# Kernel tuning notes

Hardware: AMD Instinct MI355X
Metric: run time of the kernel (lower is better)

The kernel has to match this reference:

```python
import jax, jax.numpy as jnp
import numpy as np

EPS = 1e-06
NUM_HEADS = 16
THETA = 10000.0


def rope_tables(grid_size, head_dim):
    # matches VisionRotaryEmbeddingFast: 2D rope, table shape [grid^2, head_dim]
    half = head_dim // 2
    freqs = 1.0 / THETA ** (jnp.arange(0, half, 2, dtype=jnp.float32) / half)
    freqs = jnp.concatenate([freqs, freqs], axis=0)  # [half]
    t = jnp.arange(grid_size, dtype=jnp.float32)
    f = jnp.outer(t, freqs)  # [grid, half]
    fh = jnp.broadcast_to(f[:, None, :], (grid_size, grid_size, half))
    fw = jnp.broadcast_to(f[None, :, :], (grid_size, grid_size, half))
    full = jnp.concatenate([fh, fw], axis=-1).reshape(-1, head_dim)  # [N, head_dim]
    return jnp.cos(full), jnp.sin(full)


def rotate_half(x):
    n = x.shape[-1] // 2
    return jnp.concatenate((-x[..., n:], x[..., :n]), axis=-1)


def rms_norm(x, gamma):
    var = jnp.mean(x * x, axis=-1, keepdims=True)
    return x * jax.lax.rsqrt(var + EPS) * gamma


def setup_inputs() -> dict:
    key = jax.random.key(0)
    ks = jax.random.split(key, 5)
    B, N, C = 32, 1024, 1024
    return {
        "x": jax.random.normal(ks[0], (B, N, C), dtype=jnp.float32),
        "qkv_w": jax.random.normal(ks[1], (C, 3 * C), dtype=jnp.float32) * (C ** -0.5),
        "qkv_b": jnp.zeros((3 * C,), dtype=jnp.float32),
        "proj_w": jax.random.normal(ks[2], (C, C), dtype=jnp.float32) * (C ** -0.5),
        "proj_b": jnp.zeros((C,), dtype=jnp.float32),
        "q_gamma": jnp.ones((C // NUM_HEADS,), dtype=jnp.float32),
        "k_gamma": jnp.ones((C // NUM_HEADS,), dtype=jnp.float32),
    }


def reference(x, qkv_w, qkv_b, proj_w, proj_b, q_gamma, k_gamma):
    B, N, C = x.shape
    H = NUM_HEADS
    hd = C // H
    grid = int(np.sqrt(N))
    cos, sin = rope_tables(grid, hd)  # [N, hd] each
    cos = cos[None, :, None, :]  # broadcast over [B, N, H, hd]
    sin = sin[None, :, None, :]

    qkv = (x @ qkv_w + qkv_b).reshape(B, N, 3, H, hd)
    q, k, v = qkv[:, :, 0], qkv[:, :, 1], qkv[:, :, 2]  # [B, N, H, hd]

    q = rms_norm(q, q_gamma)
    k = rms_norm(k, k_gamma)
    q = q * cos + rotate_half(q) * sin
    k = k * cos + rotate_half(k) * sin

    out = jax.nn.dot_product_attention(q, k, v, is_causal=False)  # [B, N, H, hd]
    out = out.reshape(B, N, C)
    return out @ proj_w + proj_b
```

## Files before the change

### kernel.cpp

```cpp
#include <hip/hip_runtime.h>
#include <stdint.h>

typedef float f32x4 __attribute__((ext_vector_type(4)));
typedef short s16x8 __attribute__((ext_vector_type(8)));
typedef unsigned short u16;

__device__ __forceinline__ u16 f2bf(float f) {
  union { float f; uint32_t u; } c; c.f = f;
  uint32_t u = c.u;
  u = (u + 0x7fffu + ((u >> 16) & 1u)) >> 16;
  return (u16)u;
}

__device__ __forceinline__ u16 f2bf_fast(float f) {
  union { float f; uint32_t u; } c; c.f = f;
  return (u16)((c.u + 0x8000u) >> 16);
}

__device__ __forceinline__ void gload16(const void* g, void* lds) {
  __builtin_amdgcn_global_load_lds(
      (const __attribute__((address_space(1))) void*)g,
      (__attribute__((address_space(3))) void*)lds, 16, 0, 0);
}

__device__ __forceinline__ f32x4 mfma16(s16x8 a, s16x8 b, f32x4 c) {
  return __builtin_amdgcn_mfma_f32_16x16x32_bf16(a, b, c, 0, 0, 0);
}

__device__ __forceinline__ int swz(int row, int c8) {
  return row * 64 + ((c8 ^ (row & 7)) << 3);
}

__global__ void cvt_bf16(const float* __restrict__ in, u16* __restrict__ out, size_t n) {
  size_t i = ((size_t)blockIdx.x * blockDim.x + threadIdx.x) * 4;
  if (i < n) {
    float4 v = *(const float4*)&in[i];
    u16 o0 = f2bf(v.x), o1 = f2bf(v.y), o2 = f2bf(v.z), o3 = f2bf(v.w);
    uint2 packed;
    packed.x = (uint32_t)o0 | ((uint32_t)o1 << 16);
    packed.y = (uint32_t)o2 | ((uint32_t)o3 << 16);
    *(uint2*)&out[i] = packed;
  }
}

__global__ void transpose_cvt(const float* __restrict__ in, u16* __restrict__ out,
                              int rows, int cols) {
  __shared__ float tile[64][65];
  const int c0 = blockIdx.x * 64, r0 = blockIdx.y * 64;
  const int tr = threadIdx.x >> 6, tc = threadIdx.x & 63;
#pragma unroll
  for (int i = 0; i < 16; i++) {
    int r = i * 4 + tr;
    tile[r][tc] = in[(size_t)(r0 + r) * cols + c0 + tc];
  }
  __syncthreads();
#pragma unroll
  for (int i = 0; i < 16; i++) {
    int oc = i * 4 + tr;
    out[(size_t)(c0 + oc) * rows + r0 + tc] = f2bf(tile[tc][oc]);
  }
}

__global__ void rope_tables_kernel(float* __restrict__ cosT, float* __restrict__ sinT) {
  int n = blockIdx.x;
  int d = threadIdx.x;
  int ph = n >> 5, pw = n & 31;
  int pos = (d < 32) ? ph : pw;
  int fi = d & 15;
  float freq = powf(10000.f, -(float)fi / 16.f);
  float ang = (float)pos * freq;
  cosT[n * 64 + d] = cosf(ang);
  sinT[n * 64 + d] = sinf(ang);
}


#define PH_MID \
  __builtin_amdgcn_sched_barrier(0); \
  __builtin_amdgcn_s_barrier(); \
  asm volatile("s_waitcnt lgkmcnt(0)" ::: "memory"); \
  __builtin_amdgcn_sched_barrier(0); \
  __builtin_amdgcn_s_setprio(1);

#define PH_END \
  __builtin_amdgcn_s_setprio(0); \
  __builtin_amdgcn_sched_barrier(0); \
  __builtin_amdgcn_s_barrier(); \
  __builtin_amdgcn_sched_barrier(0);

#define STAGE(ldsoff, g) do { \
    gload16((g) + (size_t)(w8 + srow) * 1024 + sc8 * 8,       &lds[(ldsoff) + w8 * 64]); \
    gload16((g) + (size_t)(w8 + srow + 64) * 1024 + sc8 * 8,  &lds[(ldsoff) + (w8 + 64) * 64]); \
  } while (0)

#define RD_A(dst, BUF, mh) \
  _Pragma("unroll") \
  for (int mi = 0; mi < 4; mi++) { \
    dst[mi][0] = *(const s16x8*)&lds[(BUF) * 32768 + arow0 + ((mh) * 64 + mi * 16) * 64 + swz0]; \
    dst[mi][1] = *(const s16x8*)&lds[(BUF) * 32768 + arow0 + ((mh) * 64 + mi * 16) * 64 + swz1]; \
  }

#define RD_B(dst, BUF, nh) \
  _Pragma("unroll") \
  for (int ni = 0; ni < 2; ni++) { \
    dst[ni][0] = *(const s16x8*)&lds[(BUF) * 32768 + 16384 + brow0 + ((nh) * 32 + ni * 16) * 64 + swz0]; \
    dst[ni][1] = *(const s16x8*)&lds[(BUF) * 32768 + 16384 + brow0 + ((nh) * 32 + ni * 16) * 64 + swz1]; \
  }

#define MFMA_QUAD(af, bfr, mh, nh) \
  _Pragma("unroll") \
  for (int mi = 0; mi < 4; mi++) \
    _Pragma("unroll") \
    for (int ni = 0; ni < 2; ni++) { \
      acc[(mh) * 4 + mi][(nh) * 2 + ni] = mfma16(af[mi][0], bfr[ni][0], acc[(mh) * 4 + mi][(nh) * 2 + ni]); \
      acc[(mh) * 4 + mi][(nh) * 2 + ni] = mfma16(af[mi][1], bfr[ni][1], acc[(mh) * 4 + mi][(nh) * 2 + ni]); \
    }

#define KTILE(BUF, KT, MODE) do { \
    s16x8 a0f[4][2], a1f[4][2], b0f[2][2], b1f[2][2]; \
     \
    RD_A(a0f, BUF, 0); \
    RD_B(b0f, BUF, 0); \
    if ((MODE) < 2) STAGE((1 - (BUF)) * 32768, Ag + (size_t)((KT) + 1) * 64); \
    PH_MID; MFMA_QUAD(a0f, b0f, 0, 0); PH_END; \
     \
    RD_B(b1f, BUF, 1); \
    if ((MODE) < 2) STAGE((1 - (BUF)) * 32768 + 8192, Ag + (size_t)128 * 1024 + ((KT) + 1) * 64); \
    PH_MID; MFMA_QUAD(a0f, b1f, 0, 1); PH_END; \
     \
    RD_A(a1f, BUF, 1); \
    if ((MODE) == 0) STAGE((BUF) * 32768 + 16384, Bg + (size_t)((KT) + 2) * 64); \
    PH_MID; MFMA_QUAD(a1f, b1f, 1, 1); PH_END; \
     \
    if ((MODE) == 0) STAGE((BUF) * 32768 + 16384 + 8192, Bg + (size_t)128 * 1024 + ((KT) + 2) * 64); \
    PH_MID; MFMA_QUAD(a1f, b0f, 1, 0); \
    __builtin_amdgcn_s_setprio(0); \
    if ((MODE) == 0) asm volatile("s_waitcnt vmcnt(4)" ::: "memory"); \
    if ((MODE) == 1) asm volatile("s_waitcnt vmcnt(0)" ::: "memory"); \
    __builtin_amdgcn_sched_barrier(0); \
    __builtin_amdgcn_s_barrier(); \
    __builtin_amdgcn_sched_barrier(0); \
  } while (0)

__device__ __forceinline__ void gemm_mainloop_8ph(
    const u16* __restrict__ Ag, const u16* __restrict__ Bg,
    u16* lds, f32x4 (&acc)[8][4])
{
  const int t = threadIdx.x;
  const int l = t & 63, w = t >> 6;
  const int wm = w & 1, wn = w >> 1;
  const int lrow = l & 15, lg = l >> 4;
  const int srow = l >> 3, sc8 = (l & 7) ^ srow;
  const int w8 = w * 8;
  const int swz0 = ((0 + lg) ^ (lrow & 7)) << 3;
  const int swz1 = ((4 + lg) ^ (lrow & 7)) << 3;
  const int arow0 = (wm * 128 + lrow) * 64;
  const int brow0 = (wn * 64 + lrow) * 64;

  STAGE(0,                 Ag);
  STAGE(8192,              Ag + (size_t)128 * 1024);
  STAGE(16384,             Bg);
  STAGE(16384 + 8192,      Bg + (size_t)128 * 1024);
  STAGE(32768 + 16384,          Bg + 64);
  STAGE(32768 + 16384 + 8192,   Bg + (size_t)128 * 1024 + 64);
  asm volatile("s_waitcnt vmcnt(4)" ::: "memory");
  __builtin_amdgcn_sched_barrier(0);
  __builtin_amdgcn_s_barrier();
  __builtin_amdgcn_sched_barrier(0);

#pragma unroll 1
  for (int kt = 0; kt < 14; kt += 2) {
    KTILE(0, kt, 0);
    KTILE(1, kt + 1, 0);
  }
  KTILE(0, 14, 1);
  KTILE(1, 15, 2);
}

__global__ __launch_bounds__(512, 2) void gemm_qkv(
    const u16* __restrict__ A,
    const u16* __restrict__ Bt,
    const float* __restrict__ bias,
    const float* __restrict__ qgam, const float* __restrict__ kgam,
    const float* __restrict__ cosT, const float* __restrict__ sinT,
    u16* __restrict__ qb, u16* __restrict__ kb, u16* __restrict__ vb)
{
  __shared__ u16 lds[65536];
  const int bid = blockIdx.x;
  const int sb = (bid & 7) * 192 + (bid >> 3);
  const int bm = sb / 12, bn = sb % 12;

  const f32x4 fzero = {0.f, 0.f, 0.f, 0.f};
  f32x4 acc[8][4];
#pragma unroll
  for (int i = 0; i < 8; i++)
#pragma unroll
    for (int j = 0; j < 4; j++) acc[i][j] = fzero;

  gemm_mainloop_8ph(A + (size_t)bm * 256 * 1024, Bt + (size_t)bn * 256 * 1024, lds, acc);

  const int t = threadIdx.x, l = t & 63, w = t >> 6;
  const int wm = w & 1, wn = w >> 1, lrow = l & 15, lg = l >> 4;
  const int colb = bn * 256 + wn * 64;
  const int s = colb >> 10;
  const int h = (colb & 1023) >> 6;

  float biasv[4], g[4];
#pragma unroll
  for (int nt = 0; nt < 4; nt++) biasv[nt] = bias[colb + nt * 16 + lrow];
  const float* gamma = (s == 0) ? qgam : kgam;
#pragma unroll
  for (int nt = 0; nt < 4; nt++) g[nt] = gamma[nt * 16 + lrow];

  if (s < 2) {
    u16* dst = (s == 0) ? qb : kb;
    const float mul = (s == 0) ? 0.18033688011112042f : 1.0f;
#pragma unroll
    for (int mf = 0; mf < 8; mf++) {
#pragma unroll
      for (int r = 0; r < 4; r++) {
        const int rowg = bm * 256 + wm * 128 + mf * 16 + lg * 4 + r;
        const int b = rowg >> 10, np = rowg & 1023;
        float tmp[4]; float sq = 0.f;
#pragma unroll
        for (int nt = 0; nt < 4; nt++) {
          float v = acc[mf][nt][r] + biasv[nt];
          tmp[nt] = v; sq += v * v;
        }
#pragma unroll
        for (int off = 1; off < 16; off <<= 1) sq += __shfl_xor(sq, off);
        const float rstd = rsqrtf(sq * 0.015625f + 1e-6f);
#pragma unroll
        for (int nt = 0; nt < 4; nt++) tmp[nt] *= rstd * g[nt];
        const size_t base = (((size_t)(b * 16 + h)) * 1024 + np) * 64;
#pragma unroll
        for (int nt = 0; nt < 4; nt++) {
          const int d = nt * 16 + lrow;
          const float cv = cosT[np * 64 + d], sv = sinT[np * 64 + d];
          const float rh = (nt < 2) ? -tmp[nt + 2] : tmp[nt - 2];
          dst[base + d] = f2bf((tmp[nt] * cv + rh * sv) * mul);
        }
      }
    }
  } else {
#pragma unroll
    for (int mf = 0; mf < 8; mf++) {
#pragma unroll
      for (int r = 0; r < 4; r++) {
        const int rowg = bm * 256 + wm * 128 + mf * 16 + lg * 4 + r;
        const int b = rowg >> 10, np = rowg & 1023;
        const size_t hb = ((size_t)(b * 16 + h)) * 64;
#pragma unroll
        for (int nt = 0; nt < 4; nt++) {
          const int d = nt * 16 + lrow;
          vb[(hb + d) * 1024 + np] = f2bf(acc[mf][nt][r] + biasv[nt]);
        }
      }
    }
  }
}

__global__ __launch_bounds__(256, 3) void attn_kernel(
    const u16* __restrict__ qbuf, const u16* __restrict__ kbuf,
    const u16* __restrict__ vtbuf, u16* __restrict__ obuf)
{
  __shared__ u16 Qs[128 * 64];
  __shared__ u16 Ks[64 * 64];
  __shared__ u16 VTs[64 * 64];
  __shared__ u16 Ps[128 * 64];
  const int bx = blockIdx.x;
  const int bh = bx >> 3, qt = bx & 7;
  const int t = threadIdx.x, l = t & 63, w = t >> 6;
  const int lrow = l & 15, lg = l >> 4;

  const u16* qg  = qbuf  + (size_t)bh * 65536 + (size_t)qt * 8192;
  const u16* kg0 = kbuf  + (size_t)bh * 65536;
  const u16* vt0 = vtbuf + (size_t)bh * 65536;

  const int srow = l >> 3;
  const int sc8  = (l & 7) ^ (srow & 7);

#pragma unroll
  for (int i = 0; i < 4; i++) {
    const int r0 = (w + i * 4) * 8;
    gload16(qg + (size_t)(r0 + srow) * 64 + sc8 * 8, &Qs[r0 * 64]);
  }
#pragma unroll
  for (int i = 0; i < 2; i++) {
    const int r0 = (w + i * 4) * 8;
    gload16(kg0 + (size_t)(r0 + srow) * 64 + sc8 * 8, &Ks[r0 * 64]);
    gload16(vt0 + (size_t)(r0 + srow) * 1024 + sc8 * 8, &VTs[r0 * 64]);
  }
  asm volatile("s_waitcnt vmcnt(0)" ::: "memory");
  __syncthreads();

  s16x8 aq[2][2];
#pragma unroll
  for (int mt = 0; mt < 2; mt++)
#pragma unroll
    for (int kh = 0; kh < 2; kh++)
      aq[mt][kh] = *(const s16x8*)&Qs[swz(w * 32 + mt * 16 + lrow, kh * 4 + lg)];

  const f32x4 fzero = {0.f, 0.f, 0.f, 0.f};
  f32x4 o[2][4];
  float l_[2][4];
#pragma unroll
  for (int mt = 0; mt < 2; mt++) {
#pragma unroll
    for (int dt = 0; dt < 4; dt++) o[mt][dt] = fzero;
#pragma unroll
    for (int r = 0; r < 4; r++) l_[mt][r] = 0.f;
  }

  for (int kt = 0; kt < 16; kt++) {
    s16x8 bk[4][2];
#pragma unroll
    for (int nt = 0; nt < 4; nt++)
#pragma unroll
      for (int kh = 0; kh < 2; kh++)
        bk[nt][kh] = *(const s16x8*)&Ks[swz(nt * 16 + lrow, kh * 4 + lg)];

    f32x4 sf[2][4];
#pragma unroll
    for (int mt = 0; mt < 2; mt++)
#pragma unroll
      for (int nt = 0; nt < 4; nt++) {
        f32x4 z = fzero;
        z = mfma16(aq[mt][0], bk[nt][0], z);
        z = mfma16(aq[mt][1], bk[nt][1], z);
        sf[mt][nt] = z;
      }

#pragma unroll
    for (int mt = 0; mt < 2; mt++) {
      const int rowb = w * 32 + mt * 16 + lg * 4;
#pragma unroll
      for (int r = 0; r < 4; r++) {
        const int row = rowb + r;
        u16* prow = &Ps[row * 64 + (lrow & 7)];
        const int rm = row & 7;
        float acc_l = 0.f;
#pragma unroll
        for (int nt = 0; nt < 4; nt++) {
          float p = __builtin_amdgcn_exp2f(sf[mt][nt][r]);
          acc_l += p;
          prow[((nt * 2 + (lrow >> 3)) ^ rm) << 3] = f2bf_fast(p);
        }
        l_[mt][r] += acc_l;
      }
    }
    asm volatile("s_waitcnt lgkmcnt(0)" ::: "memory");

    s16x8 ap[2][2], bv[4][2];
#pragma unroll
    for (int mt = 0; mt < 2; mt++)
#pragma unroll
      for (int kh = 0; kh < 2; kh++)
        ap[mt][kh] = *(const s16x8*)&Ps[swz(w * 32 + mt * 16 + lrow, kh * 4 + lg)];
#pragma unroll
    for (int dt = 0; dt < 4; dt++)
#pragma unroll
      for (int kh = 0; kh < 2; kh++)
        bv[dt][kh] = *(const s16x8*)&VTs[swz(dt * 16 + lrow, kh * 4 + lg)];
#pragma unroll
    for (int mt = 0; mt < 2; mt++)
#pragma unroll
      for (int dt = 0; dt < 4; dt++) {
        o[mt][dt] = mfma16(ap[mt][0], bv[dt][0], o[mt][dt]);
        o[mt][dt] = mfma16(ap[mt][1], bv[dt][1], o[mt][dt]);
      }

    __syncthreads();
    if (kt < 15) {
      const int kb = (kt + 1) * 64;
#pragma unroll
      for (int i = 0; i < 2; i++) {
        const int r0 = (w + i * 4) * 8;
        gload16(kg0 + (size_t)(kb + r0 + srow) * 64 + sc8 * 8, &Ks[r0 * 64]);
        gload16(vt0 + (size_t)(r0 + srow) * 1024 + kb + sc8 * 8, &VTs[r0 * 64]);
      }
      asm volatile("s_waitcnt vmcnt(0)" ::: "memory");
      __syncthreads();
    }
  }

  const int b = bh >> 4, h = bh & 15;
#pragma unroll
  for (int mt = 0; mt < 2; mt++)
#pragma unroll
    for (int r = 0; r < 4; r++) {
      float lsum = l_[mt][r];
#pragma unroll
      for (int off = 1; off < 16; off <<= 1) lsum += __shfl_xor(lsum, off);
      const float inv = 1.0f / lsum;
      const int n = qt * 128 + w * 32 + mt * 16 + lg * 4 + r;
      const size_t base = (((size_t)b * 1024 + n) * 16 + h) * 64;
#pragma unroll
      for (int dt = 0; dt < 4; dt++)
        obuf[base + dt * 16 + lrow] = f2bf(o[mt][dt][r] * inv);
    }
}

__global__ __launch_bounds__(512, 2) void gemm_proj(
    const u16* __restrict__ A,
    const u16* __restrict__ Bt,
    const float* __restrict__ bias,
    float* __restrict__ out)
{
  __shared__ u16 lds[65536];
  const int bid = blockIdx.x;
  const int sb = (bid & 7) * 64 + (bid >> 3);
  const int bm = sb >> 2, bn = sb & 3;

  const f32x4 fzero = {0.f, 0.f, 0.f, 0.f};
  f32x4 acc[8][4];
#pragma unroll
  for (int i = 0; i < 8; i++)
#pragma unroll
    for (int j = 0; j < 4; j++) acc[i][j] = fzero;

  gemm_mainloop_8ph(A + (size_t)bm * 256 * 1024, Bt + (size_t)bn * 256 * 1024, lds, acc);

  const int t = threadIdx.x, l = t & 63, w = t >> 6;
  const int wm = w & 1, wn = w >> 1, lrow = l & 15, lg = l >> 4;
  const int colb = bn * 256 + wn * 64;
  float biasv[4];
#pragma unroll
  for (int nt = 0; nt < 4; nt++) biasv[nt] = bias[colb + nt * 16 + lrow];

#pragma unroll
  for (int mf = 0; mf < 8; mf++) {
#pragma unroll
    for (int r = 0; r < 4; r++) {
      const int rowg = bm * 256 + wm * 128 + mf * 16 + lg * 4 + r;
#pragma unroll
      for (int nt = 0; nt < 4; nt++) {
        const int col = colb + nt * 16 + lrow;
        out[(size_t)rowg * 1024 + col] = acc[mf][nt][r] + biasv[nt];
      }
    }
  }
}

extern "C" void kernel_launch(void* const* d_in, const int* in_sizes, int n_in,
                              void* d_out, int out_size, void* d_ws, size_t ws_size,
                              hipStream_t stream) {
  const float* x      = (const float*)d_in[0];
  const float* qkv_w  = (const float*)d_in[1];
  const float* qkv_b  = (const float*)d_in[2];
  const float* proj_w = (const float*)d_in[3];
  const float* proj_b = (const float*)d_in[4];
  const float* q_gam  = (const float*)d_in[5];
  const float* k_gam  = (const float*)d_in[6];

  char* ws = (char*)d_ws;
  u16*   xb   = (u16*)(ws);
  u16*   qb   = (u16*)(ws + 67108864);
  u16*   kb   = (u16*)(ws + 134217728);
  u16*   vb   = (u16*)(ws + 201326592);
  u16*   wqT  = (u16*)(ws + 268435456);
  u16*   wpT  = (u16*)(ws + 274726912);
  float* cosT = (float*)(ws + 276824064);
  float* sinT = (float*)(ws + 277086208);
  u16*   attn = xb;

  cvt_bf16<<<32768, 256, 0, stream>>>(x, xb, (size_t)33554432);
  transpose_cvt<<<dim3(48, 16), 256, 0, stream>>>(qkv_w, wqT, 1024, 3072);
  transpose_cvt<<<dim3(16, 16), 256, 0, stream>>>(proj_w, wpT, 1024, 1024);
  rope_tables_kernel<<<1024, 64, 0, stream>>>(cosT, sinT);

  gemm_qkv<<<dim3(1536), dim3(512), 0, stream>>>(xb, wqT, qkv_b, q_gam, k_gam,
                                                 cosT, sinT, qb, kb, vb);
  attn_kernel<<<4096, 256, 0, stream>>>(qb, kb, vb, attn);
  gemm_proj<<<dim3(512), dim3(512), 0, stream>>>(attn, wpT, proj_b, (float*)d_out);
}
```

Baseline: 734.8 us.

## Double-buffer K/V tiles in attention and stage V transpose through LDS

The attention loop now double-buffers the K and V^T tiles, so the next tile is prefetched at the top of each iteration instead of being loaded and waited on after the compute. It also raises wave priority around the MFMA blocks and lowers the launch-bounds occupancy hint from 3 to 2 to make room for the larger LDS footprint. In the QKV epilogue, the V transpose goes through per-wave LDS tiles so it is written as coalesced 16-byte rows rather than scattered 2-byte stores. The q scale factor is also folded into gamma. The explicit vmcnt wait before using the prefetched buffer is gone, and the LDS is reused without a barrier after the GEMM mainloop, so there is a race risk. A dead loop was also left in.

```diff
diff --git a/kernel.cpp b/kernel.cpp
--- a/kernel.cpp
+++ b/kernel.cpp
@@ -204,16 +204,17 @@
   const int s = colb >> 10;
   const int h = (colb & 1023) >> 6;
 
-  float biasv[4], g[4];
+  float biasv[4];
 #pragma unroll
   for (int nt = 0; nt < 4; nt++) biasv[nt] = bias[colb + nt * 16 + lrow];
-  const float* gamma = (s == 0) ? qgam : kgam;
-#pragma unroll
-  for (int nt = 0; nt < 4; nt++) g[nt] = gamma[nt * 16 + lrow];
 
   if (s < 2) {
     u16* dst = (s == 0) ? qb : kb;
     const float mul = (s == 0) ? 0.18033688011112042f : 1.0f;
+    const float* gamma = (s == 0) ? qgam : kgam;
+    float g[4];
+#pragma unroll
+    for (int nt = 0; nt < 4; nt++) g[nt] = gamma[nt * 16 + lrow] * mul;
 #pragma unroll
     for (int mf = 0; mf < 8; mf++) {
 #pragma unroll
@@ -237,35 +238,53 @@
           const int d = nt * 16 + lrow;
           const float cv = cosT[np * 64 + d], sv = sinT[np * 64 + d];
           const float rh = (nt < 2) ? -tmp[nt + 2] : tmp[nt - 2];
-          dst[base + d] = f2bf((tmp[nt] * cv + rh * sv) * mul);
+          dst[base + d] = f2bf(tmp[nt] * cv + rh * sv);
         }
       }
     }
   } else {
+    u16* L = &lds[w * 8192];
+    const int b = bm >> 2;
+    const int np0w = (bm & 3) * 256 + wm * 128;
+    const size_t hb = ((size_t)(b * 16 + h)) * 64;
 #pragma unroll
     for (int mf = 0; mf < 8; mf++) {
-#pragma unroll
-      for (int r = 0; r < 4; r++) {
-        const int rowg = bm * 256 + wm * 128 + mf * 16 + lg * 4 + r;
-        const int b = rowg >> 10, np = rowg & 1023;
-        const size_t hb = ((size_t)(b * 16 + h)) * 64;
-#pragma unroll
-        for (int nt = 0; nt < 4; nt++) {
-          const int d = nt * 16 + lrow;
-          vb[(hb + d) * 1024 + np] = f2bf(acc[mf][nt][r] + biasv[nt]);
-        }
-      }
-    }
-  }
-}
-
-__global__ __launch_bounds__(256, 3) void attn_kernel(
+      const int c = mf * 2 + (lg >> 1);
+#pragma unroll
+      for (int nt = 0; nt < 4; nt++) {
+        const int d = nt * 16 + lrow;
+        u16 p0 = f2bf(acc[mf][nt][0] + biasv[nt]);
+        u16 p1 = f2bf(acc[mf][nt][1] + biasv[nt]);
+        u16 p2 = f2bf(acc[mf][nt][2] + biasv[nt]);
+        u16 p3 = f2bf(acc[mf][nt][3] + biasv[nt]);
+        uint2 pk;
+        pk.x = (uint32_t)p0 | ((uint32_t)p1 << 16);
+        pk.y = (uint32_t)p2 | ((uint32_t)p3 << 16);
+        *(uint2*)&L[d * 128 + ((c ^ lrow) << 3) + (lg & 1) * 4] = pk;
+      }
+    }
+#pragma unroll
+    for (int i = 0; i < 16; i++) {
+      const int d = i * 4 + lg >= 64 ? 0 : i * 4 + (l >> 4);
+      (void)d;
+    }
+#pragma unroll
+    for (int i = 0; i < 16; i++) {
+      const int dq = l >> 4, jj = l & 15;
+      const int d = i * 4 + dq;
+      s16x8 vrow = *(const s16x8*)&L[d * 128 + ((jj ^ (d & 15)) << 3)];
+      *(s16x8*)&vb[(hb + d) * 1024 + np0w + jj * 8] = vrow;
+    }
+  }
+}
+
+__global__ __launch_bounds__(256, 2) void attn_kernel(
     const u16* __restrict__ qbuf, const u16* __restrict__ kbuf,
     const u16* __restrict__ vtbuf, u16* __restrict__ obuf)
 {
   __shared__ u16 Qs[128 * 64];
-  __shared__ u16 Ks[64 * 64];
-  __shared__ u16 VTs[64 * 64];
+  __shared__ u16 Ks[2][64 * 64];
+  __shared__ u16 VTs[2][64 * 64];
   __shared__ u16 Ps[128 * 64];
   const int bx = blockIdx.x;
   const int bh = bx >> 3, qt = bx & 7;
@@ -287,8 +306,8 @@
 #pragma unroll
   for (int i = 0; i < 2; i++) {
     const int r0 = (w + i * 4) * 8;
-    gload16(kg0 + (size_t)(r0 + srow) * 64 + sc8 * 8, &Ks[r0 * 64]);
-    gload16(vt0 + (size_t)(r0 + srow) * 1024 + sc8 * 8, &VTs[r0 * 64]);
+    gload16(kg0 + (size_t)(r0 + srow) * 64 + sc8 * 8, &Ks[0][r0 * 64]);
+    gload16(vt0 + (size_t)(r0 + srow) * 1024 + sc8 * 8, &VTs[0][r0 * 64]);
   }
   asm volatile("s_waitcnt vmcnt(0)" ::: "memory");
   __syncthreads();
@@ -311,15 +330,28 @@
     for (int r = 0; r < 4; r++) l_[mt][r] = 0.f;
   }
 
+#pragma unroll 2
   for (int kt = 0; kt < 16; kt++) {
+    const int cur = kt & 1;
+    if (kt < 15) {
+      const int kb = (kt + 1) * 64;
+#pragma unroll
+      for (int i = 0; i < 2; i++) {
+        const int r0 = (w + i * 4) * 8;
+        gload16(kg0 + (size_t)(kb + r0 + srow) * 64 + sc8 * 8, &Ks[cur ^ 1][r0 * 64]);
+        gload16(vt0 + (size_t)(r0 + srow) * 1024 + kb + sc8 * 8, &VTs[cur ^ 1][r0 * 64]);
+      }
+    }
+
     s16x8 bk[4][2];
 #pragma unroll
     for (int nt = 0; nt < 4; nt++)
 #pragma unroll
       for (int kh = 0; kh < 2; kh++)
-        bk[nt][kh] = *(const s16x8*)&Ks[swz(nt * 16 + lrow, kh * 4 + lg)];
+        bk[nt][kh] = *(const s16x8*)&Ks[cur][swz(nt * 16 + lrow, kh * 4 + lg)];
 
     f32x4 sf[2][4];
+    __builtin_amdgcn_s_setprio(1);
 #pragma unroll
     for (int mt = 0; mt < 2; mt++)
 #pragma unroll
@@ -329,6 +361,7 @@
         z = mfma16(aq[mt][1], bk[nt][1], z);
         sf[mt][nt] = z;
       }
+    __builtin_amdgcn_s_setprio(0);
 
 #pragma unroll
     for (int mt = 0; mt < 2; mt++) {
@@ -360,7 +393,8 @@
     for (int dt = 0; dt < 4; dt++)
 #pragma unroll
       for (int kh = 0; kh < 2; kh++)
-        bv[dt][kh] = *(const s16x8*)&VTs[swz(dt * 16 + lrow, kh * 4 + lg)];
+        bv[dt][kh] = *(const s16x8*)&VTs[cur][swz(dt * 16 + lrow, kh * 4 + lg)];
+    __builtin_amdgcn_s_setprio(1);
 #pragma unroll
     for (int mt = 0; mt < 2; mt++)
 #pragma unroll
@@ -368,19 +402,9 @@
         o[mt][dt] = mfma16(ap[mt][0], bv[dt][0], o[mt][dt]);
         o[mt][dt] = mfma16(ap[mt][1], bv[dt][1], o[mt][dt]);
       }
+    __builtin_amdgcn_s_setprio(0);
 
     __syncthreads();
-    if (kt < 15) {
-      const int kb = (kt + 1) * 64;
-#pragma unroll
-      for (int i = 0; i < 2; i++) {
-        const int r0 = (w + i * 4) * 8;
-        gload16(kg0 + (size_t)(kb + r0 + srow) * 64 + sc8 * 8, &Ks[r0 * 64]);
-        gload16(vt0 + (size_t)(r0 + srow) * 1024 + kb + sc8 * 8, &VTs[r0 * 64]);
-      }
-      asm volatile("s_waitcnt vmcnt(0)" ::: "memory");
-      __syncthreads();
-    }
   }
 
   const int b = bh >> 4, h = bh & 15;
```

New measurement: 756.8 us. 3.0% more time.
